# Kernel optimization log

Measured on AMD Instinct MI355X. Metric: run time of the kernel, lower is better.

The kernel has to match this reference:

```python
import jax, jax.numpy as jnp
import numpy as np

N = 524288   # predicate-expression nodes
M = N // 2   # binary-formula nodes
L = 50       # self.length
VOCAB = 100  # max_embeddings
OUT = 3 * L + 5  # output_size = 155


def _attention(x, W_att, b_att):
    # x: [B, k, L]. torch Attention: softmax over the stacked-args axis, weighted sum.
    logits = jnp.einsum('bkl,lo->bko', x, W_att) + b_att   # [B, k, 1]
    a = jax.nn.softmax(logits, axis=1)
    return jnp.sum(a * x, axis=1)                           # [B, L]


def setup_inputs() -> dict:
    key = jax.random.key(0)
    ks = jax.random.split(key, 20)
    s = 0.05
    inp = {
        'pe': jax.random.normal(ks[0], (VOCAB, L), jnp.float32),
        've': jax.random.normal(ks[1], (VOCAB, L), jnp.float32),
        'oe': jax.random.normal(ks[2], (VOCAB, L), jnp.float32),
        'W_pred': jax.random.normal(ks[3], (6 * L, L), jnp.float32) * s,
        'b_pred': jax.random.normal(ks[4], (L,), jnp.float32) * s,
        'W_bin': jax.random.normal(ks[5], (3 * L, L), jnp.float32) * s,
        'b_bin': jax.random.normal(ks[6], (L,), jnp.float32) * s,
        'W_un': jax.random.normal(ks[7], (L, L), jnp.float32) * s,
        'b_un': jax.random.normal(ks[8], (L,), jnp.float32) * s,
        'W_univ': jax.random.normal(ks[9], (L, L), jnp.float32) * s,
        'b_univ': jax.random.normal(ks[10], (L,), jnp.float32) * s,
        'W_att': jax.random.normal(ks[11], (L, 1), jnp.float32) * s,
        'b_att': jax.random.normal(ks[12], (1,), jnp.float32) * s,
        'W_fin': jax.random.normal(ks[13], (L, OUT), jnp.float32) * s,
        'b_fin': jax.random.normal(ks[14], (OUT,), jnp.float32) * s,
        'pred_ids': jax.random.randint(ks[15], (N,), 0, VOCAB),
        'var_ids': jax.random.randint(ks[16], (N, 5), 0, VOCAB),
        'op_ids': jax.random.randint(ks[17], (M,), 0, VOCAB),
    }
    return inp


def reference(pe, ve, oe, W_pred, b_pred, W_bin, b_bin, W_un, b_un,
              W_univ, b_univ, W_att, b_att, W_fin, b_fin,
              pred_ids, var_ids, op_ids):
    # visit_predicate_expression, batched: [predicate_emb, 5 arg embs] -> [N, 6, L]
    args = jnp.concatenate([pe[pred_ids][:, None, :], ve[var_ids]], axis=1)
    h_pred = (jax.nn.relu(args.reshape(N, 6 * L) @ W_pred + b_pred)
              + _attention(args, W_att, b_att))                      # [N, L]

    # visit_binary_formula, batched over adjacent pairs: [left, op, right]
    ops = jnp.stack([h_pred[0::2], oe[op_ids], h_pred[1::2]], axis=1)  # [M, 3, L]
    h_bin = (jax.nn.relu(ops.reshape(M, 3 * L) @ W_bin + b_bin)
             + _attention(ops, W_att, b_att))                         # [M, L]

    # visit_unary_formula, then universal quantified formula
    h_un = jax.nn.relu(h_bin @ W_un + b_un)
    h_q = jax.nn.relu(h_un @ W_univ + b_univ)

    # final projection: forward() -> self.final(...)
    return h_q @ W_fin + b_fin  # [M, OUT]
```

## Files before the change

### kernel.cpp

```cpp
#include <hip/hip_runtime.h>
#include <hip/hip_fp16.h>

#define LDIM 50
#define MBIN 262144
#define ODIM 155
#define VOCABSZ 100

typedef _Float16 f16x4 __attribute__((ext_vector_type(4)));
typedef float    f32x4 __attribute__((ext_vector_type(4)));

#define H_T    0
#define H_PE   30000
#define H_VE   35000
#define H_TO   40000
#define H_WC   50000
#define H_WU   57424
#define H_WV   61776
#define H_WF   66128
#define F_LG   38504

#define LB_WC   118784
#define LB_WU   133632
#define LB_WV   142336
#define LB_WF   118784
#define LB_SW   140544
#define LB_OP   151040
#define LB_W0   153088
#define LB_W2   155136
#define LB_W1   157184
#define LB_BU   159232
#define LB_BV   159432
#define LB_BF   159632
#define LB_LG   160256
#define LDS_BYTES 161456

__global__ __launch_bounds__(64) void precompute_kernel(
    const float* __restrict__ pe, const float* __restrict__ ve, const float* __restrict__ oe,
    const float* __restrict__ W_pred, const float* __restrict__ b_pred,
    const float* __restrict__ W_bin, const float* __restrict__ b_bin,
    const float* __restrict__ W_un, const float* __restrict__ W_univ,
    const float* __restrict__ W_fin,
    const float* __restrict__ W_att, const float* __restrict__ b_att,
    float* __restrict__ ws)
{
    __half* wsh = (__half*)ws;
    const int bid = blockIdx.x;
    const int t = threadIdx.x;
    if (bid < 600) {
        const int s = bid / VOCABSZ, v = bid % VOCABSZ;
        if (t < LDIM) {
            const float* E = (s == 0) ? pe : ve;
            float acc = (s == 0) ? b_pred[t] : 0.0f;
            for (int e = 0; e < LDIM; ++e)
                acc += E[v*LDIM + e] * W_pred[(s*LDIM + e)*LDIM + t];
            wsh[H_T + (s*VOCABSZ + v)*LDIM + t] = __float2half_rn(acc);
        }
    } else if (bid < 700) {
        const int v = bid - 600;
        if (t < LDIM) {
            float acc = b_bin[t];
            for (int e = 0; e < LDIM; ++e)
                acc += oe[v*LDIM + e] * W_bin[(LDIM + e)*LDIM + t];
            wsh[H_TO + (v*LDIM + t)*2]     = __float2half_rn(acc);
            wsh[H_TO + (v*LDIM + t)*2 + 1] = __float2half_rn(oe[v*LDIM + t]);
        }
    } else if (bid < 800) {
        const int v = bid - 700;
        if (t < LDIM) wsh[H_PE + v*LDIM + t] = __float2half_rn(pe[v*LDIM + t]);
    } else if (bid < 900) {
        const int v = bid - 800;
        if (t < LDIM) wsh[H_VE + v*LDIM + t] = __float2half_rn(ve[v*LDIM + t]);
    } else if (bid < 905) {
        const int g = (bid - 900)*64 + t;
        if (g < 300) {
            const int which = g / VOCABSZ, v = g % VOCABSZ;
            const float* E = (which == 0) ? pe : ((which == 1) ? ve : oe);
            float acc = b_att[0];
            for (int e = 0; e < LDIM; ++e)
                acc += E[v*LDIM + e] * W_att[e];
            ws[F_LG + g] = acc;
        }
    } else if (bid == 905) {
        const int n = t;
        for (int k = 0; k < 116; ++k) {
            float val = 0.0f;
            if (n < LDIM) {
                if (k < 50)       val = W_bin[k*LDIM + n];
                else if (k < 100) val = W_bin[(100 + k - 50)*LDIM + n];
            }
            wsh[H_WC + n*116 + k] = __float2half_rn(val);
        }
    } else if (bid == 906) {
        const int n = t;
        for (int k = 0; k < 68; ++k) {
            float val = (n < LDIM && k < LDIM) ? W_un[k*LDIM + n] : 0.0f;
            wsh[H_WU + n*68 + k] = __float2half_rn(val);
        }
    } else if (bid == 907) {
        const int n = t;
        for (int k = 0; k < 68; ++k) {
            float val = (n < LDIM && k < LDIM) ? W_univ[k*LDIM + n] : 0.0f;
            wsh[H_WV + n*68 + k] = __float2half_rn(val);
        }
    } else {
        const int n = (bid - 908)*64 + t;
        if (n < 160) {
            for (int k = 0; k < 68; ++k) {
                float val = (n < ODIM && k < LDIM) ? W_fin[k*ODIM + n] : 0.0f;
                wsh[H_WF + n*68 + k] = __float2half_rn(val);
            }
        }
    }
}

__device__ __forceinline__ float2 nodeh(
    int i, int p, const int* __restrict__ v,
    float e0, const float* __restrict__ ek, float inv, const char* __restrict__ ldsraw)
{
    const __half2* T2  = (const __half2*)ldsraw;
    const __half2* pe2 = (const __half2*)(ldsraw + 60000);
    const __half2* ve2 = (const __half2*)(ldsraw + 70000);
    float2 lin = __half22float2(T2[p*25 + i]);
    float2 pv  = __half22float2(pe2[p*25 + i]);
    float nx = e0*pv.x, ny = e0*pv.y;
#pragma unroll
    for (int s = 0; s < 5; ++s) {
        float2 a = __half22float2(T2[((s+1)*VOCABSZ + v[s])*25 + i]);
        float2 b = __half22float2(ve2[v[s]*25 + i]);
        lin.x += a.x; lin.y += a.y;
        nx += ek[s]*b.x; ny += ek[s]*b.y;
    }
    return make_float2(fmaxf(lin.x, 0.0f) + nx*inv,
                       fmaxf(lin.y, 0.0f) + ny*inv);
}

__global__ __launch_bounds__(512)
void fused_kernel(
    const float* __restrict__ W_att, const float* __restrict__ b_att,
    const float* __restrict__ b_un, const float* __restrict__ b_univ,
    const float* __restrict__ b_fin,
    const int* __restrict__ pred_ids, const int* __restrict__ var_ids,
    const int* __restrict__ op_ids,
    const float* __restrict__ ws, float* __restrict__ out)
{
    __shared__ __align__(16) char ldsraw[LDS_BYTES];
    const __half* wsh = (const __half*)ws;
    const int tid = threadIdx.x;
    const int w = tid >> 6, l = tid & 63;
    const int lr = l & 15, q = l >> 4;
    const int jbase = blockIdx.x * 512;

    int*   opl = (int*)(ldsraw + LB_OP);
    float* w0l = (float*)(ldsraw + LB_W0);
    float* w2l = (float*)(ldsraw + LB_W2);
    float* w1l = (float*)(ldsraw + LB_W1);
    float* bul = (float*)(ldsraw + LB_BU);
    float* bvl = (float*)(ldsraw + LB_BV);
    float* bfl = (float*)(ldsraw + LB_BF);
    float* lgl = (float*)(ldsraw + LB_LG);

    {
        const uint4* s = (const uint4*)wsh;
        uint4* d = (uint4*)ldsraw;
        for (int i = tid; i < 5000; i += 512) d[i] = s[i];
        const uint2* sc = (const uint2*)(wsh + H_WC);
        uint2* dc = (uint2*)(ldsraw + LB_WC);
        for (int i = tid; i < 1856; i += 512) dc[i] = sc[i];
        const uint2* su = (const uint2*)(wsh + H_WU);
        uint2* du = (uint2*)(ldsraw + LB_WU);
        for (int i = tid; i < 1088; i += 512) du[i] = su[i];
        const uint2* sv = (const uint2*)(wsh + H_WV);
        uint2* dv = (uint2*)(ldsraw + LB_WV);
        for (int i = tid; i < 1088; i += 512) dv[i] = sv[i];
        if (tid < 300) lgl[tid] = ws[F_LG + tid];
        if (tid < LDIM) { bul[tid] = b_un[tid]; bvl[tid] = b_univ[tid]; }
        if (tid < ODIM) bfl[tid] = b_fin[tid];
    }
    __syncthreads();

    const int j = jbase + tid;
    int vA[5], vB[5];
    const int pA = pred_ids[2*j], pB = pred_ids[2*j+1];
#pragma unroll
    for (int s = 0; s < 5; ++s) { vA[s] = var_ids[(2*j)*5 + s]; vB[s] = var_ids[(2*j+1)*5 + s]; }
    const int op = op_ids[j];

    float ekA[5], ekB[5];
    const float e0A = __expf(lgl[pA]);
    const float e0B = __expf(lgl[pB]);
    float denA = e0A, denB = e0B;
#pragma unroll
    for (int s = 0; s < 5; ++s) {
        ekA[s] = __expf(lgl[VOCABSZ + vA[s]]); denA += ekA[s];
        ekB[s] = __expf(lgl[VOCABSZ + vB[s]]); denB += ekB[s];
    }
    const float invA = 1.0f / denA, invB = 1.0f / denB;
    const float batt = b_att[0];

    __half2 hA2[25], hB2[25];
    float lA = batt, lB = batt;
    const float2* Wa2 = (const float2*)W_att;
#pragma unroll
    for (int i = 0; i < 25; ++i) {
        float2 a = nodeh(i, pA, vA, e0A, ekA, invA, ldsraw);
        float2 b = nodeh(i, pB, vB, e0B, ekB, invB, ldsraw);
        hA2[i] = __floats2half2_rn(a.x, a.y);
        hB2[i] = __floats2half2_rn(b.x, b.y);
        const float2 wa = Wa2[i];
        lA += a.x*wa.x + a.y*wa.y;
        lB += b.x*wa.x + b.y*wa.y;
    }
    const float w0 = __expf(lA), w2 = __expf(lB);
    const float w1 = __expf(lgl[2*VOCABSZ + op]);
    const float inv2 = 1.0f / (w0 + w1 + w2);

    __syncthreads();

    {
        __half2* Hrow = (__half2*)ldsraw + tid*58;
#pragma unroll
        for (int i = 0; i < 25; ++i) Hrow[i] = hA2[i];
#pragma unroll
        for (int i = 0; i < 25; ++i) Hrow[25+i] = hB2[i];
        const __half2 z = __floats2half2_rn(0.0f, 0.0f);
#pragma unroll
        for (int i = 50; i < 58; ++i) Hrow[i] = z;
        opl[tid] = op;
        w0l[tid] = w0*inv2; w2l[tid] = w2*inv2; w1l[tid] = w1*inv2;
    }

    const _Float16* Hp  = (const _Float16*)ldsraw;
    __half*         Hw  = (__half*)ldsraw;
    f32x4 C[4][4];

    {
        const _Float16* Wcp = (const _Float16*)(ldsraw + LB_WC);
#pragma unroll
        for (int mt = 0; mt < 4; ++mt)
#pragma unroll
            for (int nt = 0; nt < 4; ++nt)
                C[mt][nt] = (f32x4){0.f, 0.f, 0.f, 0.f};
#pragma unroll
        for (int kk = 0; kk < 7; ++kk) {
            f16x4 bf[4];
#pragma unroll
            for (int nt = 0; nt < 4; ++nt)
                bf[nt] = *(const f16x4*)(Wcp + (nt*16 + lr)*116 + kk*16 + q*4);
#pragma unroll
            for (int mt = 0; mt < 4; ++mt) {
                f16x4 a = *(const f16x4*)(Hp + (w*64 + mt*16 + lr)*116 + kk*16 + q*4);
#pragma unroll
                for (int nt = 0; nt < 4; ++nt)
                    C[mt][nt] = __builtin_amdgcn_mfma_f32_16x16x16f16(a, bf[nt], C[mt][nt], 0, 0, 0);
            }
        }
        const __half2* TOg = (const __half2*)(wsh + H_TO);
#pragma unroll
        for (int mt = 0; mt < 4; ++mt)
#pragma unroll
            for (int nt = 0; nt < 4; ++nt) {
                const int d = nt*16 + lr;
#pragma unroll
                for (int r = 0; r < 4; ++r) {
                    const int node = w*64 + mt*16 + q*4 + r;
                    float v = 0.0f;
                    if (d < LDIM) {
                        const int opn = opl[node];
                        const float2 to = __half22float2(TOg[opn*LDIM + d]);
                        const float hA = __half2float(Hp[node*116 + d]);
                        const float hB = __half2float(Hp[node*116 + 50 + d]);
                        v = fmaxf(C[mt][nt][r] + to.x, 0.0f)
                          + w0l[node]*hA + w2l[node]*hB + w1l[node]*to.y;
                    }
                    C[mt][nt][r] = v;
                }
            }
    }
    __syncthreads();
#pragma unroll
    for (int mt = 0; mt < 4; ++mt)
#pragma unroll
        for (int nt = 0; nt < 4; ++nt) {
            const int d = nt*16 + lr;
#pragma unroll
            for (int r = 0; r < 4; ++r)
                Hw[(w*64 + mt*16 + q*4 + r)*68 + d] = __float2half(C[mt][nt][r]);
        }

    {
        const _Float16* Wup = (const _Float16*)(ldsraw + LB_WU);
#pragma unroll
        for (int mt = 0; mt < 4; ++mt)
#pragma unroll
            for (int nt = 0; nt < 4; ++nt)
                C[mt][nt] = (f32x4){0.f, 0.f, 0.f, 0.f};
#pragma unroll
        for (int kk = 0; kk < 4; ++kk) {
            f16x4 bf[4];
#pragma unroll
            for (int nt = 0; nt < 4; ++nt)
                bf[nt] = *(const f16x4*)(Wup + (nt*16 + lr)*68 + kk*16 + q*4);
#pragma unroll
            for (int mt = 0; mt < 4; ++mt) {
                f16x4 a = *(const f16x4*)(Hp + (w*64 + mt*16 + lr)*68 + kk*16 + q*4);
#pragma unroll
                for (int nt = 0; nt < 4; ++nt)
                    C[mt][nt] = __builtin_amdgcn_mfma_f32_16x16x16f16(a, bf[nt], C[mt][nt], 0, 0, 0);
            }
        }
    }
    __syncthreads();
    {
#pragma unroll
        for (int mt = 0; mt < 4; ++mt)
#pragma unroll
            for (int nt = 0; nt < 4; ++nt) {
                const int d = nt*16 + lr;
#pragma unroll
                for (int r = 0; r < 4; ++r) {
                    const float v = (d < LDIM) ? fmaxf(C[mt][nt][r] + bul[d], 0.0f) : 0.0f;
                    Hw[(w*64 + mt*16 + q*4 + r)*68 + d] = __float2half(v);
                }
            }
        const uint2* sf = (const uint2*)(wsh + H_WF);
        uint2* df = (uint2*)(ldsraw + LB_WF);
        for (int i = tid; i < 2720; i += 512) df[i] = sf[i];
    }

    {
        const _Float16* Wvp = (const _Float16*)(ldsraw + LB_WV);
#pragma unroll
        for (int mt = 0; mt < 4; ++mt)
#pragma unroll
            for (int nt = 0; nt < 4; ++nt)
                C[mt][nt] = (f32x4){0.f, 0.f, 0.f, 0.f};
#pragma unroll
        for (int kk = 0; kk < 4; ++kk) {
            f16x4 bf[4];
#pragma unroll
            for (int nt = 0; nt < 4; ++nt)
                bf[nt] = *(const f16x4*)(Wvp + (nt*16 + lr)*68 + kk*16 + q*4);
#pragma unroll
            for (int mt = 0; mt < 4; ++mt) {
                f16x4 a = *(const f16x4*)(Hp + (w*64 + mt*16 + lr)*68 + kk*16 + q*4);
#pragma unroll
                for (int nt = 0; nt < 4; ++nt)
                    C[mt][nt] = __builtin_amdgcn_mfma_f32_16x16x16f16(a, bf[nt], C[mt][nt], 0, 0, 0);
            }
        }
#pragma unroll
        for (int mt = 0; mt < 4; ++mt)
#pragma unroll
            for (int nt = 0; nt < 4; ++nt) {
                const int d = nt*16 + lr;
#pragma unroll
                for (int r = 0; r < 4; ++r) {
                    const float v = (d < LDIM) ? fmaxf(C[mt][nt][r] + bvl[d], 0.0f) : 0.0f;
                    Hw[(w*64 + mt*16 + q*4 + r)*68 + d] = __float2half(v);
                }
            }
    }
    __syncthreads();

    {
        const _Float16* Wfp = (const _Float16*)(ldsraw + LB_WF);
        float* sww = (float*)(ldsraw + LB_SW) + w*272;
        for (int nt = 0; nt < 10; ++nt) {
            f16x4 bf[4];
#pragma unroll
            for (int kk = 0; kk < 4; ++kk)
                bf[kk] = *(const f16x4*)(Wfp + (nt*16 + lr)*68 + kk*16 + q*4);
            const int o = nt*16 + lr;
#pragma unroll
            for (int mt = 0; mt < 4; ++mt) {
                f32x4 c = (f32x4){0.f, 0.f, 0.f, 0.f};
#pragma unroll
                for (int kk = 0; kk < 4; ++kk) {
                    f16x4 a = *(const f16x4*)(Hp + (w*64 + mt*16 + lr)*68 + kk*16 + q*4);
                    c = __builtin_amdgcn_mfma_f32_16x16x16f16(a, bf[kk], c, 0, 0, 0);
                }
#pragma unroll
                for (int r = 0; r < 4; ++r)
                    sww[(q*4 + r)*17 + lr] = c[r] + ((o < ODIM) ? bfl[o] : 0.0f);
                float* gb = out + (size_t)(jbase + w*64 + mt*16) * ODIM + nt*16;
#pragma unroll
                for (int it = 0; it < 4; ++it) {
                    const int row = it*4 + q;
                    if (nt*16 + lr < ODIM)
                        gb[row*ODIM + lr] = sww[row*17 + lr];
                }
            }
        }
    }
}

extern "C" void kernel_launch(void* const* d_in, const int* in_sizes, int n_in,
                              void* d_out, int out_size, void* d_ws, size_t ws_size,
                              hipStream_t stream) {
    const float* pe     = (const float*)d_in[0];
    const float* ve     = (const float*)d_in[1];
    const float* oe     = (const float*)d_in[2];
    const float* W_pred = (const float*)d_in[3];
    const float* b_pred = (const float*)d_in[4];
    const float* W_bin  = (const float*)d_in[5];
    const float* b_bin  = (const float*)d_in[6];
    const float* W_un   = (const float*)d_in[7];
    const float* b_un   = (const float*)d_in[8];
    const float* W_univ = (const float*)d_in[9];
    const float* b_univ = (const float*)d_in[10];
    const float* W_att  = (const float*)d_in[11];
    const float* b_att  = (const float*)d_in[12];
    const float* W_fin  = (const float*)d_in[13];
    const float* b_fin  = (const float*)d_in[14];
    const int* pred_ids = (const int*)d_in[15];
    const int* var_ids  = (const int*)d_in[16];
    const int* op_ids   = (const int*)d_in[17];
    float* out = (float*)d_out;
    float* ws  = (float*)d_ws;

    precompute_kernel<<<911, 64, 0, stream>>>(pe, ve, oe, W_pred, b_pred,
                                              W_bin, b_bin, W_un, W_univ, W_fin,
                                              W_att, b_att, ws);
    fused_kernel<<<MBIN/512, 512, 0, stream>>>(W_att, b_att, b_un, b_univ, b_fin,
                                               pred_ids, var_ids, op_ids, ws, out);
}
```

Baseline: 360.8 us.

## Pad embedding tables to 56 halves for 16-byte LDS gathers, restructure precompute

Gather tables (pred/var projections and raw pe/ve embeddings) are merged into one table with rows padded to 56 halves, so each node row is read with seven 16-byte LDS loads instead of 25 four-byte loads. Attention weights are moved into LDS, and the per-node loop is rewritten to process 8 elements per group. The precompute kernel is repacked into fewer 256-thread blocks. In exchange the table and LDS footprint grow slightly and the unrolled loop holds more values in registers.

```diff
diff --git a/kernel.cpp b/kernel.cpp
--- a/kernel.cpp
+++ b/kernel.cpp
@@ -9,15 +9,13 @@
 typedef _Float16 f16x4 __attribute__((ext_vector_type(4)));
 typedef float    f32x4 __attribute__((ext_vector_type(4)));
 
-#define H_T    0
-#define H_PE   30000
-#define H_VE   35000
-#define H_TO   40000
-#define H_WC   50000
-#define H_WU   57424
-#define H_WV   61776
-#define H_WF   66128
-#define F_LG   38504
+#define H_TBL  0
+#define H_TO   44800
+#define H_WC   54800
+#define H_WU   62224
+#define H_WV   66576
+#define H_WF   70928
+#define F_LG   40960
 
 #define LB_WC   118784
 #define LB_WU   133632
@@ -32,9 +30,10 @@
 #define LB_BV   159432
 #define LB_BF   159632
 #define LB_LG   160256
-#define LDS_BYTES 161456
-
-__global__ __launch_bounds__(64) void precompute_kernel(
+#define LB_WATT 161456
+#define LDS_BYTES 161680
+
+__global__ __launch_bounds__(256) void precompute_kernel(
     const float* __restrict__ pe, const float* __restrict__ ve, const float* __restrict__ oe,
     const float* __restrict__ W_pred, const float* __restrict__ b_pred,
     const float* __restrict__ W_bin, const float* __restrict__ b_bin,
@@ -44,94 +43,119 @@
     float* __restrict__ ws)
 {
     __half* wsh = (__half*)ws;
-    const int bid = blockIdx.x;
-    const int t = threadIdx.x;
-    if (bid < 600) {
-        const int s = bid / VOCABSZ, v = bid % VOCABSZ;
-        if (t < LDIM) {
-            const float* E = (s == 0) ? pe : ve;
-            float acc = (s == 0) ? b_pred[t] : 0.0f;
-            for (int e = 0; e < LDIM; ++e)
-                acc += E[v*LDIM + e] * W_pred[(s*LDIM + e)*LDIM + t];
-            wsh[H_T + (s*VOCABSZ + v)*LDIM + t] = __float2half_rn(acc);
-        }
-    } else if (bid < 700) {
-        const int v = bid - 600;
-        if (t < LDIM) {
+    const int bid = blockIdx.x, tid = threadIdx.x;
+    if (bid < 150) {
+        const int row = bid*4 + (tid >> 6);
+        const int t = tid & 63;
+        const int s = row / VOCABSZ, v = row % VOCABSZ;
+        if (t < 56) {
+            float acc = 0.0f;
+            if (t < 50) {
+                acc = (s == 0) ? b_pred[t] : 0.0f;
+                const float* E = (s == 0) ? pe : ve;
+#pragma unroll
+                for (int e = 0; e < 50; ++e)
+                    acc += E[v*50 + e] * W_pred[(s*50 + e)*50 + t];
+            }
+            wsh[H_TBL + row*56 + t] = __float2half_rn(acc);
+        }
+    } else if (bid < 152) {
+        const int which = bid - 150;
+        const float* E = which ? ve : pe;
+        const int base = H_TBL + (600 + which*100) * 56;
+        for (int idx = tid; idx < 5600; idx += 256) {
+            const int r = idx / 56, c = idx % 56;
+            wsh[base + idx] = __float2half_rn((c < 50) ? E[r*50 + c] : 0.0f);
+        }
+    } else if (bid < 177) {
+        const int v = (bid - 152)*4 + (tid >> 6);
+        const int t = tid & 63;
+        if (t < 50) {
             float acc = b_bin[t];
-            for (int e = 0; e < LDIM; ++e)
-                acc += oe[v*LDIM + e] * W_bin[(LDIM + e)*LDIM + t];
-            wsh[H_TO + (v*LDIM + t)*2]     = __float2half_rn(acc);
-            wsh[H_TO + (v*LDIM + t)*2 + 1] = __float2half_rn(oe[v*LDIM + t]);
-        }
-    } else if (bid < 800) {
-        const int v = bid - 700;
-        if (t < LDIM) wsh[H_PE + v*LDIM + t] = __float2half_rn(pe[v*LDIM + t]);
-    } else if (bid < 900) {
-        const int v = bid - 800;
-        if (t < LDIM) wsh[H_VE + v*LDIM + t] = __float2half_rn(ve[v*LDIM + t]);
-    } else if (bid < 905) {
-        const int g = (bid - 900)*64 + t;
-        if (g < 300) {
+#pragma unroll
+            for (int e = 0; e < 50; ++e)
+                acc += oe[v*50 + e] * W_bin[(50 + e)*50 + t];
+            wsh[H_TO + (v*50 + t)*2]     = __float2half_rn(acc);
+            wsh[H_TO + (v*50 + t)*2 + 1] = __float2half_rn(oe[v*50 + t]);
+        }
+    } else if (bid == 177) {
+        const int n = tid & 63, kc = tid >> 6;
+        for (int k = kc*29; k < kc*29 + 29; ++k) {
+            float val = 0.0f;
+            if (n < 50) {
+                if (k < 50)       val = W_bin[k*50 + n];
+                else if (k < 100) val = W_bin[(100 + k - 50)*50 + n];
+            }
+            wsh[H_WC + n*116 + k] = __float2half_rn(val);
+        }
+    } else if (bid == 178) {
+        const int n = tid & 63;
+        const int half = tid >> 7;
+        const int kc = (tid >> 6) & 1;
+        const float* W = half ? W_univ : W_un;
+        const int base = half ? H_WV : H_WU;
+        for (int k = kc*34; k < kc*34 + 34; ++k) {
+            float val = (n < 50 && k < 50) ? W[k*50 + n] : 0.0f;
+            wsh[base + n*68 + k] = __float2half_rn(val);
+        }
+    } else if (bid == 179) {
+        for (int idx = tid; idx < 10880; idx += 256) {
+            const int n = idx % 160, k = idx / 160;
+            float val = (n < ODIM && k < 50) ? W_fin[k*ODIM + n] : 0.0f;
+            wsh[H_WF + n*68 + k] = __float2half_rn(val);
+        }
+    } else {
+        for (int g = tid; g < 300; g += 256) {
             const int which = g / VOCABSZ, v = g % VOCABSZ;
             const float* E = (which == 0) ? pe : ((which == 1) ? ve : oe);
             float acc = b_att[0];
-            for (int e = 0; e < LDIM; ++e)
-                acc += E[v*LDIM + e] * W_att[e];
+#pragma unroll
+            for (int e = 0; e < 50; ++e)
+                acc += E[v*50 + e] * W_att[e];
             ws[F_LG + g] = acc;
         }
-    } else if (bid == 905) {
-        const int n = t;
-        for (int k = 0; k < 116; ++k) {
-            float val = 0.0f;
-            if (n < LDIM) {
-                if (k < 50)       val = W_bin[k*LDIM + n];
-                else if (k < 100) val = W_bin[(100 + k - 50)*LDIM + n];
-            }
-            wsh[H_WC + n*116 + k] = __float2half_rn(val);
-        }
-    } else if (bid == 906) {
-        const int n = t;
-        for (int k = 0; k < 68; ++k) {
-            float val = (n < LDIM && k < LDIM) ? W_un[k*LDIM + n] : 0.0f;
-            wsh[H_WU + n*68 + k] = __float2half_rn(val);
-        }
-    } else if (bid == 907) {
-        const int n = t;
-        for (int k = 0; k < 68; ++k) {
-            float val = (n < LDIM && k < LDIM) ? W_univ[k*LDIM + n] : 0.0f;
-            wsh[H_WV + n*68 + k] = __float2half_rn(val);
-        }
-    } else {
-        const int n = (bid - 908)*64 + t;
-        if (n < 160) {
-            for (int k = 0; k < 68; ++k) {
-                float val = (n < ODIM && k < LDIM) ? W_fin[k*ODIM + n] : 0.0f;
-                wsh[H_WF + n*68 + k] = __float2half_rn(val);
-            }
-        }
     }
 }
 
-__device__ __forceinline__ float2 nodeh(
-    int i, int p, const int* __restrict__ v,
-    float e0, const float* __restrict__ ek, float inv, const char* __restrict__ ldsraw)
+__device__ __forceinline__ float build_node(
+    int p, const int* __restrict__ v, float e0, const float* __restrict__ ek,
+    float inv, float batt, const char* __restrict__ ldsraw, __half2* __restrict__ h2)
 {
-    const __half2* T2  = (const __half2*)ldsraw;
-    const __half2* pe2 = (const __half2*)(ldsraw + 60000);
-    const __half2* ve2 = (const __half2*)(ldsraw + 70000);
-    float2 lin = __half22float2(T2[p*25 + i]);
-    float2 pv  = __half22float2(pe2[p*25 + i]);
-    float nx = e0*pv.x, ny = e0*pv.y;
-#pragma unroll
-    for (int s = 0; s < 5; ++s) {
-        float2 a = __half22float2(T2[((s+1)*VOCABSZ + v[s])*25 + i]);
-        float2 b = __half22float2(ve2[v[s]*25 + i]);
-        lin.x += a.x; lin.y += a.y;
-        nx += ek[s]*b.x; ny += ek[s]*b.y;
-    }
-    return make_float2(fmaxf(lin.x, 0.0f) + nx*inv,
-                       fmaxf(lin.y, 0.0f) + ny*inv);
+    const uint4* Tq = (const uint4*)ldsraw;
+    const float* wattl = (const float*)(ldsraw + LB_WATT);
+    float l = batt;
+#pragma unroll
+    for (int g = 0; g < 7; ++g) {
+        uint4 ul = Tq[p*7 + g];
+        uint4 up = Tq[(600 + p)*7 + g];
+        float2 lin[4], num[4];
+#pragma unroll
+        for (int k = 0; k < 4; ++k) {
+            lin[k] = __half22float2(((const __half2*)&ul)[k]);
+            float2 pp = __half22float2(((const __half2*)&up)[k]);
+            num[k] = make_float2(e0*pp.x, e0*pp.y);
+        }
+#pragma unroll
+        for (int s = 0; s < 5; ++s) {
+            uint4 ua = Tq[((s+1)*VOCABSZ + v[s])*7 + g];
+            uint4 uv = Tq[(700 + v[s])*7 + g];
+#pragma unroll
+            for (int k = 0; k < 4; ++k) {
+                float2 a = __half22float2(((const __half2*)&ua)[k]);
+                float2 b = __half22float2(((const __half2*)&uv)[k]);
+                lin[k].x += a.x; lin[k].y += a.y;
+                num[k].x += ek[s]*b.x; num[k].y += ek[s]*b.y;
+            }
+        }
+#pragma unroll
+        for (int k = 0; k < 4; ++k) {
+            const float hx = fmaxf(lin[k].x, 0.0f) + num[k].x*inv;
+            const float hy = fmaxf(lin[k].y, 0.0f) + num[k].y*inv;
+            l += hx*wattl[g*8 + 2*k] + hy*wattl[g*8 + 2*k + 1];
+            h2[g*4 + k] = __floats2half2_rn(hx, hy);
+        }
+    }
+    return __expf(l);
 }
 
 __global__ __launch_bounds__(512)
@@ -158,11 +182,12 @@
     float* bvl = (float*)(ldsraw + LB_BV);
     float* bfl = (float*)(ldsraw + LB_BF);
     float* lgl = (float*)(ldsraw + LB_LG);
+    float* wattl = (float*)(ldsraw + LB_WATT);
 
     {
         const uint4* s = (const uint4*)wsh;
         uint4* d = (uint4*)ldsraw;
-        for (int i = tid; i < 5000; i += 512) d[i] = s[i];
+        for (int i = tid; i < 5600; i += 512) d[i] = s[i];
         const uint2* sc = (const uint2*)(wsh + H_WC);
         uint2* dc = (uint2*)(ldsraw + LB_WC);
         for (int i = tid; i < 1856; i += 512) dc[i] = sc[i];
@@ -175,6 +200,7 @@
         if (tid < 300) lgl[tid] = ws[F_LG + tid];
         if (tid < LDIM) { bul[tid] = b_un[tid]; bvl[tid] = b_univ[tid]; }
         if (tid < ODIM) bfl[tid] = b_fin[tid];
+        if (tid >= 256 && tid < 312) wattl[tid-256] = (tid-256 < 50) ? W_att[tid-256] : 0.0f;
     }
     __syncthreads();
 
@@ -197,20 +223,9 @@
     const float invA = 1.0f / denA, invB = 1.0f / denB;
     const float batt = b_att[0];
 
-    __half2 hA2[25], hB2[25];
-    float lA = batt, lB = batt;
-    const float2* Wa2 = (const float2*)W_att;
-#pragma unroll
-    for (int i = 0; i < 25; ++i) {
-        float2 a = nodeh(i, pA, vA, e0A, ekA, invA, ldsraw);
-        float2 b = nodeh(i, pB, vB, e0B, ekB, invB, ldsraw);
-        hA2[i] = __floats2half2_rn(a.x, a.y);
-        hB2[i] = __floats2half2_rn(b.x, b.y);
-        const float2 wa = Wa2[i];
-        lA += a.x*wa.x + a.y*wa.y;
-        lB += b.x*wa.x + b.y*wa.y;
-    }
-    const float w0 = __expf(lA), w2 = __expf(lB);
+    __half2 hA2[28], hB2[28];
+    const float w0 = build_node(pA, vA, e0A, ekA, invA, batt, ldsraw, hA2);
+    const float w2 = build_node(pB, vB, e0B, ekB, invB, batt, ldsraw, hB2);
     const float w1 = __expf(lgl[2*VOCABSZ + op]);
     const float inv2 = 1.0f / (w0 + w1 + w2);
 
@@ -418,9 +433,9 @@
     float* out = (float*)d_out;
     float* ws  = (float*)d_ws;
 
-    precompute_kernel<<<911, 64, 0, stream>>>(pe, ve, oe, W_pred, b_pred,
-                                              W_bin, b_bin, W_un, W_univ, W_fin,
-                                              W_att, b_att, ws);
+    precompute_kernel<<<181, 256, 0, stream>>>(pe, ve, oe, W_pred, b_pred,
+                                               W_bin, b_bin, W_un, W_univ, W_fin,
+                                               W_att, b_att, ws);
     fused_kernel<<<MBIN/512, 512, 0, stream>>>(W_att, b_att, b_un, b_univ, b_fin,
                                                pred_ids, var_ids, op_ids, ws, out);
 }
```

Measured after the change: 335.1 us. 1.08x faster.
